# Optimization experiments

Hardware: AMD Instinct MI355X
Metric: run time of the kernel (lower is better)

Reference implementation:

```python
import jax, jax.numpy as jnp
import numpy as np

N = 50000      # nodes
E = 1600000    # edges (avg degree 32)
F_IN = 128
HID = 256
C = 40


def setup_inputs() -> dict:
    key = jax.random.key(0)
    ks = jax.random.split(key, 12)
    x = jax.random.normal(ks[0], (N, F_IN), jnp.float32)
    edge_index = jax.random.randint(ks[1], (2, E), 0, N, dtype=jnp.int32)

    def glorot(k, fan_in, fan_out):
        s = jnp.sqrt(2.0 / (fan_in + fan_out)).astype(jnp.float32)
        return jax.random.normal(k, (fan_in, fan_out), jnp.float32) * s

    return {
        "x": x,
        "edge_index": edge_index,
        "W1": glorot(ks[2], F_IN, HID), "b1": jnp.zeros((HID,), jnp.float32),
        "W2": glorot(ks[3], HID, HID),  "b2": jnp.zeros((HID,), jnp.float32),
        "W3": glorot(ks[4], HID, HID),  "b3": jnp.zeros((HID,), jnp.float32),
        "W4": glorot(ks[5], HID, C),    "b4": jnp.zeros((C,), jnp.float32),
    }


def _gcn_conv(x, W, b, src, dst, norm_e, self_norm):
    # PyG GCNConv: h = X W; out_j = sum_i norm_ij * h_i  (+ self-loop term) + b
    h = x @ W                                   # [N, F_out]
    msg = h[src] * norm_e[:, None]              # [E, F_out] gather + scale
    agg = jax.ops.segment_sum(msg, dst, num_segments=N)
    agg = agg + h * self_norm[:, None]          # self-loop contribution
    return agg + b


def reference(x, edge_index, W1, b1, W2, b2, W3, b3, W4, b4):
    src, dst = edge_index[0], edge_index[1]
    # degree on A + I (self-loops added), computed over destination nodes
    deg = jax.ops.segment_sum(jnp.ones((E,), x.dtype), dst, num_segments=N) + 1.0
    inv_sqrt = jax.lax.rsqrt(deg)               # [N]
    norm_e = inv_sqrt[src] * inv_sqrt[dst]      # [E] symmetric norm per edge
    self_norm = inv_sqrt * inv_sqrt             # [N] self-loop norm = 1/deg

    h = jax.nn.relu(_gcn_conv(x, W1, b1, src, dst, norm_e, self_norm))
    h = jax.nn.relu(_gcn_conv(h, W2, b2, src, dst, norm_e, self_norm))
    h = jax.nn.relu(_gcn_conv(h, W3, b3, src, dst, norm_e, self_norm))
    h = _gcn_conv(h, W4, b4, src, dst, norm_e, self_norm)
    return jax.nn.log_softmax(h, axis=1)
```

## Files before the change

### kernel.cpp

```cpp
#include <hip/hip_runtime.h>
#include <hip/hip_fp16.h>
#include <math.h>


typedef _Float16 f16x8 __attribute__((ext_vector_type(8)));
typedef float f32x4 __attribute__((ext_vector_type(4)));

#define SB 8
#define SBSHIFT 13

__device__ __forceinline__ __half2 u2h2(unsigned u) {
    union { unsigned u; __half2 h; } v; v.u = u; return v.h;
}
__device__ __forceinline__ unsigned h22u(__half2 h) {
    union { unsigned u; __half2 h; } v; v.h = h; return v.u;
}
__device__ __forceinline__ float hlo(unsigned u) {
    return __half2float(__ushort_as_half((unsigned short)(u & 0xFFFFu)));
}
__device__ __forceinline__ float hhi(unsigned u) {
    return __half2float(__ushort_as_half((unsigned short)(u >> 16)));
}


__global__ __launch_bounds__(256) void count_kernel(const int* __restrict__ src,
                                                    const int* __restrict__ dst,
                                                    int* __restrict__ counts,
                                                    int* __restrict__ rank, int E) {
    int e = blockIdx.x * 256 + threadIdx.x;
    if (e < E) {
        int d = dst[e], s = src[e];
        rank[e] = atomicAdd(&counts[d * SB + (s >> SBSHIFT)], 1);
    }
}

__global__ __launch_bounds__(256) void scan_phase1(const int* __restrict__ counts,
                                                   int* __restrict__ blockSums, int NS) {
    int i = blockIdx.x * 256 + threadIdx.x;
    int v = (i < NS) ? counts[i] : 0;
    #pragma unroll
    for (int o = 32; o >= 1; o >>= 1) v += __shfl_xor(v, o, 64);
    __shared__ int ws[4];
    int lane = threadIdx.x & 63, w = threadIdx.x >> 6;
    if (lane == 0) ws[w] = v;
    __syncthreads();
    if (threadIdx.x == 0) blockSums[blockIdx.x] = ws[0] + ws[1] + ws[2] + ws[3];
}

__global__ __launch_bounds__(1024) void scan_phase2(int* __restrict__ bs, int nb) {
    __shared__ int s[1024];
    int tid = threadIdx.x;
    int v0 = (2 * tid < nb) ? bs[2 * tid] : 0;
    int v1 = (2 * tid + 1 < nb) ? bs[2 * tid + 1] : 0;
    int ps = v0 + v1;
    s[tid] = ps;
    __syncthreads();
    for (int off = 1; off < 1024; off <<= 1) {
        int t = (tid >= off) ? s[tid - off] : 0;
        __syncthreads();
        s[tid] += t;
        __syncthreads();
    }
    int excl = s[tid] - ps;
    if (2 * tid < nb) bs[2 * tid] = excl;
    if (2 * tid + 1 < nb) bs[2 * tid + 1] = excl + v0;
}

__global__ __launch_bounds__(256) void scan_phase3(const int* __restrict__ counts,
                                                   const int* __restrict__ blockSums,
                                                   int* __restrict__ offs2, int NS) {
    __shared__ int s[256];
    int tid = threadIdx.x;
    int i = blockIdx.x * 256 + tid;
    int c = (i < NS) ? counts[i] : 0;
    s[tid] = c;
    __syncthreads();
    for (int off = 1; off < 256; off <<= 1) {
        int t = (tid >= off) ? s[tid - off] : 0;
        __syncthreads();
        s[tid] += t;
        __syncthreads();
    }
    if (i < NS) {
        int excl = s[tid] - c + blockSums[blockIdx.x];
        offs2[i] = excl;
        if (i == NS - 1) offs2[NS] = excl + c;
    }
}

__global__ __launch_bounds__(256) void finalize_kernel(const int* __restrict__ offs2,
                                                       int* __restrict__ offs,
                                                       float* __restrict__ rsq, int N) {
    int n = blockIdx.x * 256 + threadIdx.x;
    if (n < N) {
        int b0 = offs2[n * SB];
        int b1 = offs2[n * SB + SB];
        offs[n] = b0;
        rsq[n] = rsqrtf((float)(b1 - b0) + 1.0f);
        if (n == N - 1) offs[N] = b1;
    }
}

__global__ __launch_bounds__(256) void scatter_kernel(const int* __restrict__ src,
                                                      const int* __restrict__ dst,
                                                      const int* __restrict__ rank,
                                                      const int* __restrict__ offs2,
                                                      const float* __restrict__ rsq,
                                                      unsigned* __restrict__ epk, int E) {
    int e = blockIdx.x * 256 + threadIdx.x;
    if (e < E) {
        int d = dst[e];
        int s = src[e];
        int pos = offs2[d * SB + (s >> SBSHIFT)] + rank[e];
        float w = rsq[s] * rsq[d];
        epk[pos] = (unsigned)s |
                   ((unsigned)__half_as_ushort(__float2half_rn(w)) << 16);
    }
}

__global__ __launch_bounds__(256) void prep_kernel(
        const float* __restrict__ x, unsigned short* __restrict__ xb, int nx4,
        const float* __restrict__ W1, const float* __restrict__ W2,
        const float* __restrict__ W3, const float* __restrict__ W4,
        unsigned short* __restrict__ Wt1, unsigned short* __restrict__ Wt2,
        unsigned short* __restrict__ Wt3, unsigned short* __restrict__ Wt4) {
    int i = blockIdx.x * 256 + threadIdx.x;
    if (i < nx4) {
        float4 v = reinterpret_cast<const float4*>(x)[i];
        ushort4 o;
        o.x = __half_as_ushort(__float2half_rn(v.x));
        o.y = __half_as_ushort(__float2half_rn(v.y));
        o.z = __half_as_ushort(__float2half_rn(v.z));
        o.w = __half_as_ushort(__float2half_rn(v.w));
        reinterpret_cast<ushort4*>(xb)[i] = o;
        return;
    }
    int j = i - nx4;
    if (j < 32768) {
        int k = j >> 8, n = j & 255;
        Wt1[n * 128 + k] = __half_as_ushort(__float2half_rn(W1[j]));
    } else if (j < 98304) {
        int t = j - 32768; int k = t >> 8, n = t & 255;
        Wt2[n * 256 + k] = __half_as_ushort(__float2half_rn(W2[t]));
    } else if (j < 163840) {
        int t = j - 98304; int k = t >> 8, n = t & 255;
        Wt3[n * 256 + k] = __half_as_ushort(__float2half_rn(W3[t]));
    } else if (j < 174080) {
        int t = j - 163840; int k = t / 40, n = t - k * 40;
        Wt4[n * 256 + k] = __half_as_ushort(__float2half_rn(W4[t]));
    }
}

template <int ROWU, bool BIAS, bool RELU>
__global__ __launch_bounds__(256) void agg_pass_kernel(
        const unsigned* __restrict__ G,
        const int* __restrict__ offs,
        const unsigned* __restrict__ epk,
        const float* __restrict__ rsq,
        const float* __restrict__ bias,
        unsigned* __restrict__ out, int N, int colOff) {
    constexpr int UNR = 8;
    int lane = threadIdx.x & 63;
    int node = blockIdx.x * 4 + (threadIdx.x >> 6);
    if (node >= N) return;
    const unsigned* base = G + colOff + lane;

    __half2 acc = u2h2(0u);
    int e = offs[node], e1 = offs[node + 1];
    for (; e + UNR - 1 < e1; e += UNR) {
        unsigned p[UNR];
        int s[UNR];
        #pragma unroll
        for (int j = 0; j < UNR; j++) { p[j] = epk[e + j]; s[j] = p[j] & 0xFFFFu; }
        unsigned g[UNR];
        #pragma unroll
        for (int j = 0; j < UNR; j++) g[j] = base[(size_t)s[j] * ROWU];
        #pragma unroll
        for (int j = 0; j < UNR; j++) {
            __half2 w2 = __half2half2(__ushort_as_half((unsigned short)(p[j] >> 16)));
            acc = __hfma2(w2, u2h2(g[j]), acc);
        }
    }
    for (; e < e1; e++) {
        unsigned p0 = epk[e];
        int s0 = p0 & 0xFFFFu;
        __half2 w2 = __half2half2(__ushort_as_half((unsigned short)(p0 >> 16)));
        acc = __hfma2(w2, u2h2(base[(size_t)s0 * ROWU]), acc);
    }

    float sn = rsq[node];
    sn *= sn;
    unsigned sv = base[(size_t)node * ROWU];
    float2 f = __half22float2(acc);
    f.x = fmaf(sn, hlo(sv), f.x);
    f.y = fmaf(sn, hhi(sv), f.y);
    if (BIAS) {
        float2 b = reinterpret_cast<const float2*>(bias)[colOff + lane];
        f.x += b.x; f.y += b.y;
    }
    if (RELU) { f.x = fmaxf(f.x, 0.f); f.y = fmaxf(f.y, 0.f); }
    out[(size_t)node * ROWU + colOff + lane] = h22u(__floats2half2_rn(f.x, f.y));
}

__global__ __launch_bounds__(256) void agg40_softmax_kernel(
        const unsigned* __restrict__ G,
        const int* __restrict__ offs,
        const unsigned* __restrict__ epk,
        const float* __restrict__ rsq,
        const float* __restrict__ bias,
        float* __restrict__ out, int N) {
    int lane = threadIdx.x & 63;
    int node = blockIdx.x * 4 + (threadIdx.x >> 6);
    if (node >= N) return;
    bool act = lane < 20;
    int cl = act ? lane : 0;
    __half2 acch = u2h2(0u);
    int e = offs[node], e1 = offs[node + 1];
    for (; e + 3 < e1; e += 4) {
        unsigned p[4];
        int s[4];
        #pragma unroll
        for (int j = 0; j < 4; j++) { p[j] = epk[e + j]; s[j] = p[j] & 0xFFFFu; }
        unsigned g[4];
        #pragma unroll
        for (int j = 0; j < 4; j++) g[j] = G[(size_t)s[j] * 20 + cl];
        #pragma unroll
        for (int j = 0; j < 4; j++) {
            __half2 w = __half2half2(__ushort_as_half((unsigned short)(p[j] >> 16)));
            acch = __hfma2(w, u2h2(g[j]), acch);
        }
    }
    for (; e < e1; e++) {
        unsigned p0 = epk[e];
        int s0 = p0 & 0xFFFFu;
        __half2 w0 = __half2half2(__ushort_as_half((unsigned short)(p0 >> 16)));
        acch = __hfma2(w0, u2h2(G[(size_t)s0 * 20 + cl]), acch);
    }
    float lo = 0.f, hi = 0.f;
    if (act) {
        float sn = rsq[node];
        sn *= sn;
        unsigned sv = G[(size_t)node * 20 + lane];
        float2 f = __half22float2(acch);
        lo = fmaf(sn, hlo(sv), f.x) + bias[2 * lane];
        hi = fmaf(sn, hhi(sv), f.y) + bias[2 * lane + 1];
    }
    float m = act ? fmaxf(lo, hi) : -INFINITY;
    #pragma unroll
    for (int o = 32; o >= 1; o >>= 1) m = fmaxf(m, __shfl_xor(m, o, 64));
    float s = act ? (expf(lo - m) + expf(hi - m)) : 0.f;
    #pragma unroll
    for (int o = 32; o >= 1; o >>= 1) s += __shfl_xor(s, o, 64);
    float ls = logf(s);
    if (act) {
        float2 o2;
        o2.x = lo - m - ls;
        o2.y = hi - m - ls;
        *reinterpret_cast<float2*>(out + (size_t)node * 40 + 2 * lane) = o2;
    }
}

template <bool BIAS, bool RELU>
__global__ __launch_bounds__(256) void gemm_f16(
        const unsigned short* __restrict__ A,
        const unsigned short* __restrict__ Bt,
        const float* __restrict__ bias,
        unsigned short* __restrict__ Cout,
        int M, int K, int Nc) {
    __shared__ __align__(16) unsigned short As[128 * 72];
    __shared__ __align__(16) unsigned short Bs[128 * 72];
    int tid = threadIdx.x;
    int lane = tid & 63;
    int wid = tid >> 6;
    int rowBase = blockIdx.y * 128;
    int colBase = blockIdx.x * 128;
    int waveM = (wid & 1) * 64;
    int waveN = (wid >> 1) * 64;

    f32x4 acc[4][4] = {};
    int lrow = lane & 15;
    int kgrp = (lane >> 4) * 8;

    for (int k0 = 0; k0 < K; k0 += 64) {
        #pragma unroll
        for (int i = 0; i < 4; i++) {
            int c = tid + 256 * i;
            int row = c >> 3;
            int kp = (c & 7) * 8;
            int4 av = make_int4(0, 0, 0, 0);
            int gr = rowBase + row;
            if (gr < M)
                av = *reinterpret_cast<const int4*>(A + (size_t)gr * K + k0 + kp);
            *reinterpret_cast<int4*>(&As[row * 72 + kp]) = av;
            int4 bv = make_int4(0, 0, 0, 0);
            int gc = colBase + row;
            if (gc < Nc)
                bv = *reinterpret_cast<const int4*>(Bt + (size_t)gc * K + k0 + kp);
            *reinterpret_cast<int4*>(&Bs[row * 72 + kp]) = bv;
        }
        __syncthreads();
        #pragma unroll
        for (int kk = 0; kk < 64; kk += 32) {
            f16x8 af[4], bfr[4];
            #pragma unroll
            for (int t = 0; t < 4; t++) {
                af[t] = *reinterpret_cast<const f16x8*>(
                    &As[(waveM + t * 16 + lrow) * 72 + kk + kgrp]);
                bfr[t] = *reinterpret_cast<const f16x8*>(
                    &Bs[(waveN + t * 16 + lrow) * 72 + kk + kgrp]);
            }
            #pragma unroll
            for (int mt = 0; mt < 4; mt++)
                #pragma unroll
                for (int nt = 0; nt < 4; nt++)
                    acc[mt][nt] = __builtin_amdgcn_mfma_f32_16x16x32_f16(
                        af[mt], bfr[nt], acc[mt][nt], 0, 0, 0);
        }
        __syncthreads();
    }

    #pragma unroll
    for (int mt = 0; mt < 4; mt++) {
        #pragma unroll
        for (int r = 0; r < 4; r++) {
            int row = rowBase + waveM + mt * 16 + (lane >> 4) * 4 + r;
            if (row >= M) continue;
            #pragma unroll
            for (int nt = 0; nt < 4; nt++) {
                int col = colBase + waveN + nt * 16 + (lane & 15);
                if (col >= Nc) continue;
                float v = acc[mt][nt][r];
                if (BIAS) v += bias[col];
                if (RELU) v = fmaxf(v, 0.f);
                Cout[(size_t)row * Nc + col] = __half_as_ushort(__float2half_rn(v));
            }
        }
    }
}


extern "C" void kernel_launch(void* const* d_in, const int* in_sizes, int n_in,
                              void* d_out, int out_size, void* d_ws, size_t ws_size,
                              hipStream_t stream) {
    const float* x  = (const float*)d_in[0];
    const int*   ei = (const int*)d_in[1];
    const float* W1 = (const float*)d_in[2];
    const float* b1 = (const float*)d_in[3];
    const float* W2 = (const float*)d_in[4];
    const float* b2 = (const float*)d_in[5];
    const float* W3 = (const float*)d_in[6];
    const float* b3 = (const float*)d_in[7];
    const float* W4 = (const float*)d_in[8];
    const float* b4 = (const float*)d_in[9];

    const int FIN = 128, HID = 256, C = 40;
    const int N = in_sizes[0] / FIN;
    const int E = in_sizes[1] / 2;
    const int* src = ei;
    const int* dst = ei + E;
    const int NS = N * SB;

    char* w = (char*)d_ws;
    auto alloc = [&](size_t bytes) {
        char* p = w;
        w += (bytes + 255) & ~(size_t)255;
        return p;
    };
    int nScanBlocks = (NS + 255) / 256;
    int*   counts = (int*)alloc((size_t)NS * 4);
    int*   offs2  = (int*)alloc((size_t)(NS + 1) * 4);
    int*   offs   = (int*)alloc((size_t)(N + 1) * 4);
    float* rsq    = (float*)alloc((size_t)N * 4);
    int*   bsums  = (int*)alloc((size_t)nScanBlocks * 4);
    int*   rank   = (int*)alloc((size_t)E * 4);
    unsigned* epk = (unsigned*)alloc((size_t)E * 4);
    unsigned short* xb   = (unsigned short*)alloc((size_t)N * FIN * 2);
    unsigned short* aggx = (unsigned short*)alloc((size_t)N * FIN * 2);
    unsigned short* bufA = (unsigned short*)alloc((size_t)N * HID * 2);
    unsigned short* bufB = (unsigned short*)alloc((size_t)N * HID * 2);
    unsigned short* Wt1 = (unsigned short*)alloc((size_t)FIN * HID * 2);
    unsigned short* Wt2 = (unsigned short*)alloc((size_t)HID * HID * 2);
    unsigned short* Wt3 = (unsigned short*)alloc((size_t)HID * HID * 2);
    unsigned short* Wt4 = (unsigned short*)alloc((size_t)HID * C * 2);

    hipMemsetAsync(counts, 0, (size_t)NS * 4, stream);

    int nx4 = N * FIN / 4;
    prep_kernel<<<(nx4 + 174080 + 255) / 256, 256, 0, stream>>>(
        x, xb, nx4, W1, W2, W3, W4, Wt1, Wt2, Wt3, Wt4);

    count_kernel<<<(E + 255) / 256, 256, 0, stream>>>(src, dst, counts, rank, E);
    scan_phase1<<<nScanBlocks, 256, 0, stream>>>(counts, bsums, NS);
    scan_phase2<<<1, 1024, 0, stream>>>(bsums, nScanBlocks);
    scan_phase3<<<nScanBlocks, 256, 0, stream>>>(counts, bsums, offs2, NS);
    finalize_kernel<<<(N + 255) / 256, 256, 0, stream>>>(offs2, offs, rsq, N);
    scatter_kernel<<<(E + 255) / 256, 256, 0, stream>>>(src, dst, rank, offs2, rsq,
                                                        epk, E);

    int grp = (N + 3) / 4;
    dim3 gHID((HID + 127) / 128, (N + 127) / 128);
    dim3 gC((C + 127) / 128, (N + 127) / 128);

    agg_pass_kernel<64, false, false>
        <<<grp, 256, 0, stream>>>((const unsigned*)xb, offs, epk, rsq, nullptr,
                                  (unsigned*)aggx, N, 0);
    gemm_f16<true, true><<<gHID, 256, 0, stream>>>(aggx, Wt1, b1, bufA, N, FIN, HID);
    gemm_f16<false, false><<<gHID, 256, 0, stream>>>(bufA, Wt2, nullptr, bufB,
                                                     N, HID, HID);
    agg_pass_kernel<128, true, true>
        <<<grp, 256, 0, stream>>>((const unsigned*)bufB, offs, epk, rsq, b2,
                                  (unsigned*)bufA, N, 0);
    agg_pass_kernel<128, true, true>
        <<<grp, 256, 0, stream>>>((const unsigned*)bufB, offs, epk, rsq, b2,
                                  (unsigned*)bufA, N, 64);
    gemm_f16<false, false><<<gHID, 256, 0, stream>>>(bufA, Wt3, nullptr, bufB,
                                                     N, HID, HID);
    agg_pass_kernel<128, true, true>
        <<<grp, 256, 0, stream>>>((const unsigned*)bufB, offs, epk, rsq, b3,
                                  (unsigned*)bufA, N, 0);
    agg_pass_kernel<128, true, true>
        <<<grp, 256, 0, stream>>>((const unsigned*)bufB, offs, epk, rsq, b3,
                                  (unsigned*)bufA, N, 64);
    gemm_f16<false, false><<<gC, 256, 0, stream>>>(bufA, Wt4, nullptr, bufB,
                                                   N, HID, C);
    agg40_softmax_kernel<<<grp, 256, 0, stream>>>((const unsigned*)bufB, offs, epk,
                                                  rsq, b4, (float*)d_out, N);
}
```

Measured before the change: 638.5 us.

## Replicate count buckets across 8 copies and DMA GEMM tiles into swizzled LDS

The CSR build now spreads atomic counters over 8 per-block-group copies, chosen by block index, to reduce atomic contention. The scan kernels are reworked to process 4 elements per thread over the interleaved copy layout. The count and offset arrays are aliased onto the unused layer buffers. Separately, the GEMM tile loads switch from register-staged copies to global_load_lds direct-to-LDS transfers with an XOR-swizzled layout that replaces padding for bank-conflict avoidance. The swizzle adds index arithmetic, and the scan now covers 8x more entries.

Measured after the change: 635.5 us. About the same (-0.5%).

```diff
diff --git a/kernel.cpp b/kernel.cpp
--- a/kernel.cpp
+++ b/kernel.cpp
@@ -8,6 +8,17 @@
 
 #define SB 8
 #define SBSHIFT 13
+#define NCOPY 8
+
+#define AS1 __attribute__((address_space(1)))
+#define AS3 __attribute__((address_space(3)))
+
+__device__ __forceinline__ void dma16(const unsigned short* g,
+                                      const unsigned short* ldsBase) {
+    __builtin_amdgcn_global_load_lds((const AS1 void*)(size_t)g,
+                                     (AS3 void*)(unsigned)(size_t)ldsBase,
+                                     16, 0, 0);
+}
 
 __device__ __forceinline__ __half2 u2h2(unsigned u) {
     union { unsigned u; __half2 h; } v; v.u = u; return v.h;
@@ -25,24 +36,32 @@
 
 __global__ __launch_bounds__(256) void count_kernel(const int* __restrict__ src,
                                                     const int* __restrict__ dst,
-                                                    int* __restrict__ counts,
-                                                    int* __restrict__ rank, int E) {
+                                                    int* __restrict__ cntP,
+                                                    int* __restrict__ rank,
+                                                    int E, int NS) {
     int e = blockIdx.x * 256 + threadIdx.x;
+    int c = blockIdx.x & (NCOPY - 1);
     if (e < E) {
         int d = dst[e], s = src[e];
-        rank[e] = atomicAdd(&counts[d * SB + (s >> SBSHIFT)], 1);
-    }
-}
-
-__global__ __launch_bounds__(256) void scan_phase1(const int* __restrict__ counts,
-                                                   int* __restrict__ blockSums, int NS) {
-    int i = blockIdx.x * 256 + threadIdx.x;
-    int v = (i < NS) ? counts[i] : 0;
-    #pragma unroll
-    for (int o = 32; o >= 1; o >>= 1) v += __shfl_xor(v, o, 64);
+        rank[e] = atomicAdd(&cntP[c * NS + d * SB + (s >> SBSHIFT)], 1);
+    }
+}
+
+__global__ __launch_bounds__(256) void scan_phase1(const int* __restrict__ cntP,
+                                                   int* __restrict__ blockSums,
+                                                   int NS, int NT) {
+    int base = blockIdx.x * 1024 + threadIdx.x * 4;
+    int s = 0;
+    #pragma unroll
+    for (int j = 0; j < 4; j++) {
+        int i = base + j;
+        if (i < NT) s += cntP[(i & 7) * NS + (i >> 3)];
+    }
+    #pragma unroll
+    for (int o = 32; o >= 1; o >>= 1) s += __shfl_xor(s, o, 64);
     __shared__ int ws[4];
     int lane = threadIdx.x & 63, w = threadIdx.x >> 6;
-    if (lane == 0) ws[w] = v;
+    if (lane == 0) ws[w] = s;
     __syncthreads();
     if (threadIdx.x == 0) blockSums[blockIdx.x] = ws[0] + ws[1] + ws[2] + ws[3];
 }
@@ -50,9 +69,13 @@
 __global__ __launch_bounds__(1024) void scan_phase2(int* __restrict__ bs, int nb) {
     __shared__ int s[1024];
     int tid = threadIdx.x;
-    int v0 = (2 * tid < nb) ? bs[2 * tid] : 0;
-    int v1 = (2 * tid + 1 < nb) ? bs[2 * tid + 1] : 0;
-    int ps = v0 + v1;
+    int v[4]; int ps = 0;
+    #pragma unroll
+    for (int j = 0; j < 4; j++) {
+        int i = tid * 4 + j;
+        v[j] = (i < nb) ? bs[i] : 0;
+        ps += v[j];
+    }
     s[tid] = ps;
     __syncthreads();
     for (int off = 1; off < 1024; off <<= 1) {
@@ -62,18 +85,28 @@
         __syncthreads();
     }
     int excl = s[tid] - ps;
-    if (2 * tid < nb) bs[2 * tid] = excl;
-    if (2 * tid + 1 < nb) bs[2 * tid + 1] = excl + v0;
-}
-
-__global__ __launch_bounds__(256) void scan_phase3(const int* __restrict__ counts,
+    #pragma unroll
+    for (int j = 0; j < 4; j++) {
+        int i = tid * 4 + j;
+        if (i < nb) { bs[i] = excl; excl += v[j]; }
+    }
+}
+
+__global__ __launch_bounds__(256) void scan_phase3(const int* __restrict__ cntP,
                                                    const int* __restrict__ blockSums,
-                                                   int* __restrict__ offs2, int NS) {
+                                                   int* __restrict__ offs3,
+                                                   int NS, int NT) {
     __shared__ int s[256];
     int tid = threadIdx.x;
-    int i = blockIdx.x * 256 + tid;
-    int c = (i < NS) ? counts[i] : 0;
-    s[tid] = c;
+    int base = blockIdx.x * 1024 + tid * 4;
+    int c[4]; int ps = 0;
+    #pragma unroll
+    for (int j = 0; j < 4; j++) {
+        int i = base + j;
+        c[j] = (i < NT) ? cntP[(i & 7) * NS + (i >> 3)] : 0;
+        ps += c[j];
+    }
+    s[tid] = ps;
     __syncthreads();
     for (int off = 1; off < 256; off <<= 1) {
         int t = (tid >= off) ? s[tid - off] : 0;
@@ -81,20 +114,25 @@
         s[tid] += t;
         __syncthreads();
     }
-    if (i < NS) {
-        int excl = s[tid] - c + blockSums[blockIdx.x];
-        offs2[i] = excl;
-        if (i == NS - 1) offs2[NS] = excl + c;
-    }
-}
-
-__global__ __launch_bounds__(256) void finalize_kernel(const int* __restrict__ offs2,
+    int excl = s[tid] - ps + blockSums[blockIdx.x];
+    #pragma unroll
+    for (int j = 0; j < 4; j++) {
+        int i = base + j;
+        if (i < NT) {
+            offs3[i] = excl;
+            excl += c[j];
+            if (i == NT - 1) offs3[NT] = excl;
+        }
+    }
+}
+
+__global__ __launch_bounds__(256) void finalize_kernel(const int* __restrict__ offs3,
                                                        int* __restrict__ offs,
                                                        float* __restrict__ rsq, int N) {
     int n = blockIdx.x * 256 + threadIdx.x;
     if (n < N) {
-        int b0 = offs2[n * SB];
-        int b1 = offs2[n * SB + SB];
+        int b0 = offs3[n * (SB * NCOPY)];
+        int b1 = offs3[(n + 1) * (SB * NCOPY)];
         offs[n] = b0;
         rsq[n] = rsqrtf((float)(b1 - b0) + 1.0f);
         if (n == N - 1) offs[N] = b1;
@@ -104,14 +142,15 @@
 __global__ __launch_bounds__(256) void scatter_kernel(const int* __restrict__ src,
                                                       const int* __restrict__ dst,
                                                       const int* __restrict__ rank,
-                                                      const int* __restrict__ offs2,
+                                                      const int* __restrict__ offs3,
                                                       const float* __restrict__ rsq,
                                                       unsigned* __restrict__ epk, int E) {
     int e = blockIdx.x * 256 + threadIdx.x;
+    int c = blockIdx.x & (NCOPY - 1);
     if (e < E) {
         int d = dst[e];
         int s = src[e];
-        int pos = offs2[d * SB + (s >> SBSHIFT)] + rank[e];
+        int pos = offs3[d * (SB * NCOPY) + (s >> SBSHIFT) * NCOPY + c] + rank[e];
         float w = rsq[s] * rsq[d];
         epk[pos] = (unsigned)s |
                    ((unsigned)__half_as_ushort(__float2half_rn(w)) << 16);
@@ -267,8 +306,8 @@
         const float* __restrict__ bias,
         unsigned short* __restrict__ Cout,
         int M, int K, int Nc) {
-    __shared__ __align__(16) unsigned short As[128 * 72];
-    __shared__ __align__(16) unsigned short Bs[128 * 72];
+    __shared__ __align__(16) unsigned short As[128 * 64];
+    __shared__ __align__(16) unsigned short Bs[128 * 64];
     int tid = threadIdx.x;
     int lane = tid & 63;
     int wid = tid >> 6;
@@ -283,20 +322,16 @@
 
     for (int k0 = 0; k0 < K; k0 += 64) {
         #pragma unroll
-        for (int i = 0; i < 4; i++) {
-            int c = tid + 256 * i;
-            int row = c >> 3;
-            int kp = (c & 7) * 8;
-            int4 av = make_int4(0, 0, 0, 0);
-            int gr = rowBase + row;
-            if (gr < M)
-                av = *reinterpret_cast<const int4*>(A + (size_t)gr * K + k0 + kp);
-            *reinterpret_cast<int4*>(&As[row * 72 + kp]) = av;
-            int4 bv = make_int4(0, 0, 0, 0);
-            int gc = colBase + row;
-            if (gc < Nc)
-                bv = *reinterpret_cast<const int4*>(Bt + (size_t)gc * K + k0 + kp);
-            *reinterpret_cast<int4*>(&Bs[row * 72 + kp]) = bv;
+        for (int c = 0; c < 4; c++) {
+            int base16 = c * 256 + wid * 64;
+            int slot = base16 + lane;
+            int row = slot >> 3;
+            int kp = (slot & 7) * 8;
+            int ksw = kp ^ ((row & 7) * 8);
+            int gr = rowBase + row; if (gr >= M) gr = M - 1;
+            dma16(A + (size_t)gr * K + k0 + ksw, &As[base16 * 8]);
+            int gc = colBase + row; if (gc >= Nc) gc = Nc - 1;
+            dma16(Bt + (size_t)gc * K + k0 + ksw, &Bs[base16 * 8]);
         }
         __syncthreads();
         #pragma unroll
@@ -304,10 +339,12 @@
             f16x8 af[4], bfr[4];
             #pragma unroll
             for (int t = 0; t < 4; t++) {
+                int ra = waveM + t * 16 + lrow;
                 af[t] = *reinterpret_cast<const f16x8*>(
-                    &As[(waveM + t * 16 + lrow) * 72 + kk + kgrp]);
+                    &As[ra * 64 + ((kk + kgrp) ^ ((ra & 7) * 8))]);
+                int rb = waveN + t * 16 + lrow;
                 bfr[t] = *reinterpret_cast<const f16x8*>(
-                    &Bs[(waveN + t * 16 + lrow) * 72 + kk + kgrp]);
+                    &Bs[rb * 64 + ((kk + kgrp) ^ ((rb & 7) * 8))]);
             }
             #pragma unroll
             for (int mt = 0; mt < 4; mt++)
@@ -359,6 +396,7 @@
     const int* src = ei;
     const int* dst = ei + E;
     const int NS = N * SB;
+    const int NT = N * SB * NCOPY;
 
     char* w = (char*)d_ws;
     auto alloc = [&](size_t bytes) {
@@ -366,9 +404,7 @@
         w += (bytes + 255) & ~(size_t)255;
         return p;
     };
-    int nScanBlocks = (NS + 255) / 256;
-    int*   counts = (int*)alloc((size_t)NS * 4);
-    int*   offs2  = (int*)alloc((size_t)(NS + 1) * 4);
+    int nScanBlocks = (NT + 1023) / 1024;
     int*   offs   = (int*)alloc((size_t)(N + 1) * 4);
     float* rsq    = (float*)alloc((size_t)N * 4);
     int*   bsums  = (int*)alloc((size_t)nScanBlocks * 4);
@@ -383,18 +419,21 @@
     unsigned short* Wt3 = (unsigned short*)alloc((size_t)HID * HID * 2);
     unsigned short* Wt4 = (unsigned short*)alloc((size_t)HID * C * 2);
 
-    hipMemsetAsync(counts, 0, (size_t)NS * 4, stream);
+    int* cntP  = (int*)bufA;
+    int* offs3 = (int*)bufB;
+
+    hipMemsetAsync(cntP, 0, (size_t)NT * 4, stream);
 
     int nx4 = N * FIN / 4;
     prep_kernel<<<(nx4 + 174080 + 255) / 256, 256, 0, stream>>>(
         x, xb, nx4, W1, W2, W3, W4, Wt1, Wt2, Wt3, Wt4);
 
-    count_kernel<<<(E + 255) / 256, 256, 0, stream>>>(src, dst, counts, rank, E);
-    scan_phase1<<<nScanBlocks, 256, 0, stream>>>(counts, bsums, NS);
+    count_kernel<<<(E + 255) / 256, 256, 0, stream>>>(src, dst, cntP, rank, E, NS);
+    scan_phase1<<<nScanBlocks, 256, 0, stream>>>(cntP, bsums, NS, NT);
     scan_phase2<<<1, 1024, 0, stream>>>(bsums, nScanBlocks);
-    scan_phase3<<<nScanBlocks, 256, 0, stream>>>(counts, bsums, offs2, NS);
-    finalize_kernel<<<(N + 255) / 256, 256, 0, stream>>>(offs2, offs, rsq, N);
-    scatter_kernel<<<(E + 255) / 256, 256, 0, stream>>>(src, dst, rank, offs2, rsq,
+    scan_phase3<<<nScanBlocks, 256, 0, stream>>>(cntP, bsums, offs3, NS, NT);
+    finalize_kernel<<<(N + 255) / 256, 256, 0, stream>>>(offs3, offs, rsq, N);
+    scatter_kernel<<<(E + 255) / 256, 256, 0, stream>>>(src, dst, rank, offs3, rsq,
                                                         epk, E);
 
     int grp = (N + 3) / 4;
```
